# Performance work log

Hardware: AMD Instinct MI355X
Metric: run time of the kernel (lower is better)

Reference implementation:

```python
import jax, jax.numpy as jnp
import numpy as np

B, D, K, E = 4096, 2048, 512, 8  # tokens, model dim, kept SVD rank, experts


def setup_inputs() -> dict:
    key = jax.random.key(0)
    ks = jax.random.split(key, 7)
    x = jax.random.normal(ks[0], (B, D), dtype=jnp.float32)
    # frozen base weight (stands in for pretrained_weight)
    W = jax.random.normal(ks[1], (D, D), dtype=jnp.float32) / np.sqrt(D)
    # frozen truncated SVD factors: U_k (D,K) left vecs, V_k (K,D) as sliced in the torch code
    U_k = jnp.linalg.qr(jax.random.normal(ks[2], (D, K), dtype=jnp.float32))[0]
    V_k = jnp.linalg.qr(jax.random.normal(ks[3], (D, K), dtype=jnp.float32))[0].T
    lambda_k = jax.random.normal(ks[4], (E, K), dtype=jnp.float32) * 0.02
    v = jnp.zeros((D,), dtype=jnp.float32)
    router_W1 = jax.random.normal(ks[5], (K, 1), dtype=jnp.float32)
    router_W2 = jax.random.normal(ks[6], (1, E), dtype=jnp.float32)
    return {"x": x, "W": W, "U_k": U_k, "V_k": V_k, "lambda_k": lambda_k,
            "v": v, "router_W1": router_W1, "router_W2": router_W2}


def reference(x, W, U_k, V_k, lambda_k, v, router_W1, router_W2):
    # routing: x @ U_k -> rank-1 router -> softmax over experts
    routing = x @ U_k                                   # (B,K)
    g = jax.nn.softmax((routing @ router_W1) @ router_W2, axis=-1)  # (B,E)
    # per-expert low-rank delta weight, materialized as in the original
    delta_W = jnp.einsum('dk,ek,kn->edn', U_k, lambda_k, V_k)       # (E,D,D)
    W_tot = W[None] + delta_W                           # (E,D,D)
    # F.linear semantics: out = x @ W_tot^T per expert
    expert_out = jnp.einsum('bd,end->ben', x, W_tot)    # (B,E,D)
    out = jnp.einsum('ben,be->bn', expert_out, g)       # gated combine
    return out * (1.0 + v)
```

## Files before the change

### kernel.cpp

```cpp
#include <hip/hip_runtime.h>
#include <hip/hip_bf16.h>
#include <cstdint>

#define B_TOK 4096
#define DDIM  2048
#define KR    512
#define NE    8

using f32x4  = __attribute__((ext_vector_type(4))) float;
using short8 = __attribute__((ext_vector_type(8))) short;
using u16 = unsigned short;

__device__ inline u16 f2bf(float f) {
    union { float f; uint32_t u; } x; x.f = f;
    uint32_t u = x.u;
    return (u16)((u + 0x7fffu + ((u >> 16) & 1u)) >> 16);
}
__device__ inline float bf2f(u16 h) {
    union { uint32_t u; float f; } x; x.u = ((uint32_t)h) << 16;
    return x.f;
}

__device__ inline void gload_lds16(const u16* g, u16* l) {
    __builtin_amdgcn_global_load_lds(
        (const __attribute__((address_space(1))) void*)g,
        (__attribute__((address_space(3))) void*)l, 16, 0, 0);
}

template<int COLS4, int SRC_LD, int DST_LD>
__device__ inline void cvt_region(const float* __restrict__ src,
                                  u16* __restrict__ dst, int i) {
    int r = i / COLS4, c = i - r * COLS4;
    float4 val = *((const float4*)(src + (size_t)r * SRC_LD) + c);
    ushort4 o;
    o.x = f2bf(val.x); o.y = f2bf(val.y); o.z = f2bf(val.z); o.w = f2bf(val.w);
    *(ushort4*)(dst + (size_t)r * DST_LD + c * 4) = o;
}

__global__ __launch_bounds__(256)
void prep_all(const float* __restrict__ x, const float* __restrict__ U,
              const float* __restrict__ V, const float* __restrict__ W1,
              u16* __restrict__ Aaug, u16* __restrict__ Vb) {
    constexpr int NB_COPY = 1024;
    constexpr int N_X = 4096 * 512;
    constexpr int N_V = 512 * 512;
    constexpr int N_Z = 63 * 512;
    constexpr int N_TOT = N_X + N_V + N_Z;
    int b = blockIdx.x;
    if (b < NB_COPY) {
        for (int i = b * 256 + threadIdx.x; i < N_TOT; i += NB_COPY * 256) {
            if (i < N_X)            cvt_region<512, 2048, 2560>(x, Aaug, i);
            else if (i < N_X + N_V) cvt_region<512, 2048, 2048>(V, Vb, i - N_X);
            else {
                int z = i - (N_X + N_V);
                ushort4 zz; zz.x = 0; zz.y = 0; zz.z = 0; zz.w = 0;
                *(ushort4*)(Vb + (size_t)513 * 2048 + (size_t)z * 4) = zz;
            }
        }
    } else {
        int wrow = (b - NB_COPY) * 4 + (threadIdx.x >> 6);
        int lane = threadIdx.x & 63;
        const float* row = U + (size_t)wrow * KR;
        float s = 0.f;
        #pragma unroll
        for (int k = 0; k < KR; k += 64) s += row[k + lane] * W1[k + lane];
        #pragma unroll
        for (int o = 32; o > 0; o >>= 1) s += __shfl_down(s, o);
        if (lane == 0) Vb[(size_t)512 * 2048 + wrow] = f2bf(s);
    }
}

__global__ __launch_bounds__(256)
void router3(const u16* __restrict__ tb, const float* __restrict__ W2,
             const float* __restrict__ lam, u16* __restrict__ Am) {
    int row = blockIdx.x, tid = threadIdx.x;
    const u16* tr = tb + (size_t)row * 576;
    float s = bf2f(tr[512]);

    float g[NE]; float mx = -1e30f;
    #pragma unroll
    for (int e = 0; e < NE; e++) { g[e] = s * W2[e]; mx = fmaxf(mx, g[e]); }
    float den = 0.f;
    #pragma unroll
    for (int e = 0; e < NE; e++) { g[e] = expf(g[e] - mx); den += g[e]; }
    float inv = 1.0f / den;

    #pragma unroll
    for (int kk = tid; kk < KR; kk += 256) {
        float mu = 0.f;
        #pragma unroll
        for (int e = 0; e < NE; e++) mu += g[e] * lam[e * KR + kk];
        Am[(size_t)row * 2560 + 2048 + kk] = f2bf(mu * inv * bf2f(tr[kk]));
    }
}

template<int BM, int BN, int WGM, int WGN, int NCOMP, bool OUT_BF16>
__global__ __launch_bounds__(256, 2)
void gemm_db(const u16* __restrict__ A, const u16* __restrict__ Bm,
             void* __restrict__ Cv,
             const float* __restrict__ Wsrc, const float* __restrict__ Usrc,
             u16* __restrict__ BigB,
             int N, int Kc, int lda, int ldb, int nbx) {
    constexpr int MF = BM / (WGM * 16);
    constexpr int NF = BN / (WGN * 16);
    constexpr int ISSA = BM / 32;
    constexpr int ISSB = BN / 32;
    __shared__ u16 sA[2 * BM * 64];
    __shared__ u16 sB[2 * BN * 64];

    if (blockIdx.x >= NCOMP) {
        constexpr int N_W = 2048 * 512;
        constexpr int N_U = 2048 * 128;
        int cb = blockIdx.x - NCOMP;
        for (int i = cb * 256 + threadIdx.x; i < N_W + N_U; i += 256 * 256) {
            if (i < N_W) cvt_region<512, 2048, 2560>(Wsrc, BigB, i);
            else         cvt_region<128, 512, 2560>(Usrc, BigB + 2048, i - N_W);
        }
        return;
    }

    const int tid = threadIdx.x;
    const int wid = tid >> 6, lane = tid & 63;
    const int l15 = lane & 15, l4 = lane >> 4;
    const int wm = wid / WGN, wn = wid % WGN;

    const int id = ((int)blockIdx.x & 7) * (NCOMP >> 3) + ((int)blockIdx.x >> 3);
    const int row0 = (id / nbx) * BM;
    const int col0 = (id % nbx) * BN;

    const int srow = tid >> 3;
    const int scol = ((tid & 7) ^ (srow & 7)) << 3;
    const u16* gA = A + (size_t)(row0 + srow) * lda + scol;
    const u16* gB = Bm + (size_t)(col0 + srow) * ldb + scol;

    f32x4 acc[MF][NF] = {};
    const int nt = Kc >> 6;

    #pragma unroll
    for (int i = 0; i < ISSA; i++)
        gload_lds16(gA + (size_t)i * 32 * lda, sA + i * 2048 + wid * 512);
    #pragma unroll
    for (int i = 0; i < ISSB; i++)
        gload_lds16(gB + (size_t)i * 32 * ldb, sB + i * 2048 + wid * 512);
    __syncthreads();

    for (int t = 0; t < nt; ++t) {
        const int cur = t & 1;
        if (t + 1 < nt) {
            const int nxt = cur ^ 1;
            const u16* gAk = gA + (size_t)(t + 1) * 64;
            const u16* gBk = gB + (size_t)(t + 1) * 64;
            #pragma unroll
            for (int i = 0; i < ISSA; i++)
                gload_lds16(gAk + (size_t)i * 32 * lda,
                            sA + nxt * BM * 64 + i * 2048 + wid * 512);
            #pragma unroll
            for (int i = 0; i < ISSB; i++)
                gload_lds16(gBk + (size_t)i * 32 * ldb,
                            sB + nxt * BN * 64 + i * 2048 + wid * 512);
        }
        const u16* a0 = sA + cur * BM * 64;
        const u16* b0 = sB + cur * BN * 64;
        #pragma unroll
        for (int kc = 0; kc < 8; kc += 4) {
            short8 af[MF], bv[NF];
            #pragma unroll
            for (int mf = 0; mf < MF; mf++) {
                int row = wm * MF * 16 + mf * 16 + l15;
                int ch = (kc + l4) ^ (row & 7);
                af[mf] = *(const short8*)(a0 + row * 64 + ch * 8);
            }
            #pragma unroll
            for (int nf = 0; nf < NF; nf++) {
                int row = wn * NF * 16 + nf * 16 + l15;
                int ch = (kc + l4) ^ (row & 7);
                bv[nf] = *(const short8*)(b0 + row * 64 + ch * 8);
            }
            #pragma unroll
            for (int mf = 0; mf < MF; mf++)
                #pragma unroll
                for (int nf = 0; nf < NF; nf++)
                    acc[mf][nf] = __builtin_amdgcn_mfma_f32_16x16x32_bf16(
                        af[mf], bv[nf], acc[mf][nf], 0, 0, 0);
        }
        __syncthreads();
    }

    #pragma unroll
    for (int nf = 0; nf < NF; nf++) {
        int col = col0 + wn * NF * 16 + nf * 16 + l15;
        #pragma unroll
        for (int mf = 0; mf < MF; mf++) {
            int row = row0 + wm * MF * 16 + mf * 16 + l4 * 4;
            #pragma unroll
            for (int r2 = 0; r2 < 4; r2++) {
                float val = acc[mf][nf][r2];
                if constexpr (OUT_BF16)
                    ((u16*)Cv)[(size_t)(row + r2) * N + col] = f2bf(val);
                else
                    ((float*)Cv)[(size_t)(row + r2) * N + col] = val;
            }
        }
    }
}

template<bool HAS_V>
__global__ __launch_bounds__(512, 1)
void gemm_ring(const u16* __restrict__ A, const u16* __restrict__ Bm,
               float* __restrict__ C, const float* __restrict__ v,
               int N, int Kc, int lda, int ldb) {
    constexpr int BM = 256, BN = 128, WGN = 2;
    constexpr int MF = 4, NF = 4;
    constexpr int SLOT = (BM + BN) * 64;
    constexpr int ROWS = 64;
    constexpr int ISSA = 4, ISSB = 2;
    __shared__ u16 lds[3 * SLOT];

    const int tid = threadIdx.x;
    const int wid = tid >> 6, lane = tid & 63;
    const int l15 = lane & 15, l4 = lane >> 4;
    const int wm = wid / WGN, wn = wid % WGN;

    const int xcd = blockIdx.x & 7;
    const int j = blockIdx.x >> 3;
    const int row0 = ((xcd >> 1) * 4 + (j >> 3)) * BM;
    const int col0 = ((xcd & 1) * 8 + (j & 7)) * BN;

    const int srow = tid >> 3;
    const int scol = ((tid & 7) ^ (srow & 7)) << 3;
    const u16* gA = A + (size_t)(row0 + srow) * lda + scol;
    const u16* gB = Bm + (size_t)(col0 + srow) * ldb + scol;

    int aoff[2][MF], boff[2][NF];
    #pragma unroll
    for (int kc = 0; kc < 2; kc++) {
        #pragma unroll
        for (int mf = 0; mf < MF; mf++) {
            int row = wm * MF * 16 + mf * 16 + l15;
            aoff[kc][mf] = row * 64 + (((kc * 4) + l4) ^ (row & 7)) * 8;
        }
        #pragma unroll
        for (int nf = 0; nf < NF; nf++) {
            int row = wn * NF * 16 + nf * 16 + l15;
            boff[kc][nf] = BM * 64 + row * 64 + (((kc * 4) + l4) ^ (row & 7)) * 8;
        }
    }

    f32x4 acc[MF][NF] = {};
    const int nt = Kc >> 6;

    #pragma unroll
    for (int p = 0; p < 2; p++) {
        const u16* gAt = gA + p * 64;
        const u16* gBt = gB + p * 64;
        u16* sl = lds + p * SLOT;
        #pragma unroll
        for (int i = 0; i < ISSA; i++)
            gload_lds16(gAt + (size_t)i * ROWS * lda,
                        sl + i * ROWS * 64 + wid * 512);
        #pragma unroll
        for (int i = 0; i < ISSB; i++)
            gload_lds16(gBt + (size_t)i * ROWS * ldb,
                        sl + BM * 64 + i * ROWS * 64 + wid * 512);
    }
    asm volatile("s_waitcnt vmcnt(6)" ::: "memory");
    __builtin_amdgcn_s_barrier();
    asm volatile("" ::: "memory");

    int sc = 0, sp = 2;
    for (int t = 0; t < nt; ++t) {
        if (t + 2 < nt) {
            const u16* gAt = gA + (size_t)(t + 2) * 64;
            const u16* gBt = gB + (size_t)(t + 2) * 64;
            u16* sl = lds + sp * SLOT;
            #pragma unroll
            for (int i = 0; i < ISSA; i++)
                gload_lds16(gAt + (size_t)i * ROWS * lda,
                            sl + i * ROWS * 64 + wid * 512);
            #pragma unroll
            for (int i = 0; i < ISSB; i++)
                gload_lds16(gBt + (size_t)i * ROWS * ldb,
                            sl + BM * 64 + i * ROWS * 64 + wid * 512);
        }
        const u16* s0 = lds + sc * SLOT;
        __builtin_amdgcn_s_setprio(1);
        #pragma unroll
        for (int kc = 0; kc < 2; kc++) {
            short8 af[MF], bv[NF];
            #pragma unroll
            for (int mf = 0; mf < MF; mf++)
                af[mf] = *(const short8*)(s0 + aoff[kc][mf]);
            #pragma unroll
            for (int nf = 0; nf < NF; nf++)
                bv[nf] = *(const short8*)(s0 + boff[kc][nf]);
            #pragma unroll
            for (int mf = 0; mf < MF; mf++)
                #pragma unroll
                for (int nf = 0; nf < NF; nf++)
                    acc[mf][nf] = __builtin_amdgcn_mfma_f32_16x16x32_bf16(
                        af[mf], bv[nf], acc[mf][nf], 0, 0, 0);
        }
        __builtin_amdgcn_s_setprio(0);

        const int rem = nt - 1 - t;
        if (rem == 0) break;
        if (rem >= 2) asm volatile("s_waitcnt vmcnt(6)" ::: "memory");
        else          asm volatile("s_waitcnt vmcnt(0)" ::: "memory");
        __builtin_amdgcn_s_barrier();
        asm volatile("" ::: "memory");
        sc = (sc == 2) ? 0 : sc + 1;
        sp = (sp == 2) ? 0 : sp + 1;
    }

    #pragma unroll
    for (int nf = 0; nf < NF; nf++) {
        int col = col0 + wn * NF * 16 + nf * 16 + l15;
        float sc2 = HAS_V ? (1.0f + v[col]) : 1.0f;
        #pragma unroll
        for (int mf = 0; mf < MF; mf++) {
            int row = row0 + wm * MF * 16 + mf * 16 + l4 * 4;
            #pragma unroll
            for (int r2 = 0; r2 < 4; r2++)
                C[(size_t)(row + r2) * N + col] = acc[mf][nf][r2] * sc2;
        }
    }
}

extern "C" void kernel_launch(void* const* d_in, const int* in_sizes, int n_in,
                              void* d_out, int out_size, void* d_ws, size_t ws_size,
                              hipStream_t stream) {
    const float* x   = (const float*)d_in[0];
    const float* W   = (const float*)d_in[1];
    const float* U   = (const float*)d_in[2];
    const float* V   = (const float*)d_in[3];
    const float* lam = (const float*)d_in[4];
    const float* v   = (const float*)d_in[5];
    const float* W1  = (const float*)d_in[6];
    const float* W2  = (const float*)d_in[7];
    float* out = (float*)d_out;

    char* ws = (char*)d_ws;
    u16* Aaug  = (u16*)ws;
    u16* BigB  = (u16*)(ws + 20971520);
    u16* Vb    = (u16*)(ws + 31457280);
    u16* tmatb = (u16*)(ws + 33816576);

    prep_all<<<1536, 256, 0, stream>>>(x, U, V, W1, Aaug, Vb);

    gemm_db<128, 64, 4, 1, 288, true><<<544, 256, 0, stream>>>(
        Aaug, Vb, tmatb, W, U, BigB, 576, 2048, 2560, 2048, 9);

    router3<<<4096, 256, 0, stream>>>(tmatb, W2, lam, Aaug);

    gemm_ring<true><<<256, 512, 0, stream>>>(
        Aaug, BigB, out, v, 2048, 2560, 2560, 2560);
}
```

Measured before the change: 95.22 us.

## Fuse fp32-to-bf16 conversion of x into the routing GEMM's A staging

Drops the separate pass in prep_all that converted x to bf16 into the augmented A buffer. The first GEMM now reads x as fp32 directly, converts it in registers and writes the bf16 tile to LDS. Blocks in the first column tile also write the converted tile out to Aaug for later kernels. This removes one full read and write pass over x, but the A staging becomes synchronous register loads instead of async global-to-LDS loads, which may stall the double-buffer pipeline.

```diff
diff --git a/kernel.cpp b/kernel.cpp
--- a/kernel.cpp
+++ b/kernel.cpp
@@ -38,21 +38,18 @@
 }
 
 __global__ __launch_bounds__(256)
-void prep_all(const float* __restrict__ x, const float* __restrict__ U,
-              const float* __restrict__ V, const float* __restrict__ W1,
-              u16* __restrict__ Aaug, u16* __restrict__ Vb) {
-    constexpr int NB_COPY = 1024;
-    constexpr int N_X = 4096 * 512;
+void prep_all(const float* __restrict__ U, const float* __restrict__ V,
+              const float* __restrict__ W1, u16* __restrict__ Vb) {
+    constexpr int NB_COPY = 256;
     constexpr int N_V = 512 * 512;
     constexpr int N_Z = 63 * 512;
-    constexpr int N_TOT = N_X + N_V + N_Z;
+    constexpr int N_TOT = N_V + N_Z;
     int b = blockIdx.x;
     if (b < NB_COPY) {
         for (int i = b * 256 + threadIdx.x; i < N_TOT; i += NB_COPY * 256) {
-            if (i < N_X)            cvt_region<512, 2048, 2560>(x, Aaug, i);
-            else if (i < N_X + N_V) cvt_region<512, 2048, 2048>(V, Vb, i - N_X);
+            if (i < N_V) cvt_region<512, 2048, 2048>(V, Vb, i);
             else {
-                int z = i - (N_X + N_V);
+                int z = i - N_V;
                 ushort4 zz; zz.x = 0; zz.y = 0; zz.z = 0; zz.w = 0;
                 *(ushort4*)(Vb + (size_t)513 * 2048 + (size_t)z * 4) = zz;
             }
@@ -96,11 +93,11 @@
 
 template<int BM, int BN, int WGM, int WGN, int NCOMP, bool OUT_BF16>
 __global__ __launch_bounds__(256, 2)
-void gemm_db(const u16* __restrict__ A, const u16* __restrict__ Bm,
+void gemm_db(const float* __restrict__ Af, const u16* __restrict__ Bm,
              void* __restrict__ Cv,
              const float* __restrict__ Wsrc, const float* __restrict__ Usrc,
-             u16* __restrict__ BigB,
-             int N, int Kc, int lda, int ldb, int nbx) {
+             u16* __restrict__ BigB, u16* __restrict__ Aout,
+             int N, int Kc, int lda , int ldb, int nbx) {
     constexpr int MF = BM / (WGM * 16);
     constexpr int NF = BN / (WGN * 16);
     constexpr int ISSA = BM / 32;
@@ -127,37 +124,48 @@
     const int id = ((int)blockIdx.x & 7) * (NCOMP >> 3) + ((int)blockIdx.x >> 3);
     const int row0 = (id / nbx) * BM;
     const int col0 = (id % nbx) * BN;
+    const bool wrA = (col0 == 0);
 
     const int srow = tid >> 3;
     const int scol = ((tid & 7) ^ (srow & 7)) << 3;
-    const u16* gA = A + (size_t)(row0 + srow) * lda + scol;
     const u16* gB = Bm + (size_t)(col0 + srow) * ldb + scol;
 
     f32x4 acc[MF][NF] = {};
     const int nt = Kc >> 6;
 
-    #pragma unroll
-    for (int i = 0; i < ISSA; i++)
-        gload_lds16(gA + (size_t)i * 32 * lda, sA + i * 2048 + wid * 512);
-    #pragma unroll
-    for (int i = 0; i < ISSB; i++)
-        gload_lds16(gB + (size_t)i * 32 * ldb, sB + i * 2048 + wid * 512);
+    auto stageA = [&](int kt, int buf) {
+        #pragma unroll
+        for (int i = 0; i < ISSA; i++) {
+            const int arow = row0 + srow + i * 32;
+            const float* src = Af + (size_t)arow * lda + kt + scol;
+            float4 f0 = *(const float4*)src;
+            float4 f1 = *(const float4*)(src + 4);
+            short8 hv;
+            hv[0] = (short)f2bf(f0.x); hv[1] = (short)f2bf(f0.y);
+            hv[2] = (short)f2bf(f0.z); hv[3] = (short)f2bf(f0.w);
+            hv[4] = (short)f2bf(f1.x); hv[5] = (short)f2bf(f1.y);
+            hv[6] = (short)f2bf(f1.z); hv[7] = (short)f2bf(f1.w);
+            *(short8*)(sA + buf * BM * 64 + i * 2048 + wid * 512 + (lane << 3)) = hv;
+            if (wrA)
+                *(short8*)(Aout + (size_t)arow * 2560 + kt + scol) = hv;
+        }
+    };
+    auto stageB = [&](int kt, int buf) {
+        #pragma unroll
+        for (int i = 0; i < ISSB; i++)
+            gload_lds16(gB + (size_t)i * 32 * ldb + kt,
+                        sB + buf * BN * 64 + i * 2048 + wid * 512);
+    };
+
+    stageB(0, 0);
+    stageA(0, 0);
     __syncthreads();
 
     for (int t = 0; t < nt; ++t) {
         const int cur = t & 1;
         if (t + 1 < nt) {
-            const int nxt = cur ^ 1;
-            const u16* gAk = gA + (size_t)(t + 1) * 64;
-            const u16* gBk = gB + (size_t)(t + 1) * 64;
-            #pragma unroll
-            for (int i = 0; i < ISSA; i++)
-                gload_lds16(gAk + (size_t)i * 32 * lda,
-                            sA + nxt * BM * 64 + i * 2048 + wid * 512);
-            #pragma unroll
-            for (int i = 0; i < ISSB; i++)
-                gload_lds16(gBk + (size_t)i * 32 * ldb,
-                            sB + nxt * BN * 64 + i * 2048 + wid * 512);
+            stageB((t + 1) * 64, cur ^ 1);
+            stageA((t + 1) * 64, cur ^ 1);
         }
         const u16* a0 = sA + cur * BM * 64;
         const u16* b0 = sB + cur * BN * 64;
@@ -345,10 +353,10 @@
     u16* Vb    = (u16*)(ws + 31457280);
     u16* tmatb = (u16*)(ws + 33816576);
 
-    prep_all<<<1536, 256, 0, stream>>>(x, U, V, W1, Aaug, Vb);
+    prep_all<<<768, 256, 0, stream>>>(U, V, W1, Vb);
 
     gemm_db<128, 64, 4, 1, 288, true><<<544, 256, 0, stream>>>(
-        Aaug, Vb, tmatb, W, U, BigB, 576, 2048, 2560, 2048, 9);
+        x, Vb, tmatb, W, U, BigB, Aaug, 576, 2048, 2048, 2048, 9);
 
     router3<<<4096, 256, 0, stream>>>(tmatb, W2, lam, Aaug);
 
```

Result: slower. 124.1 us (+30.3%).
